# Performance work log

Hardware: AMD Instinct MI355X
Metric: run time of the kernel (lower is better)

Reference implementation:

```python
import jax, jax.numpy as jnp
import numpy as np

EPS = 1e-8
H, DH = 4, 8
HID = H * DH  # 32
FF = 20       # 4 * dim
C = 5         # channels per degree


def snorm(x):
    # grad-safe L2 norm over last axis
    return jnp.sqrt(jnp.sum(x * x, axis=-1) + 1e-12)


def _ln(v, gamma, beta):
    mu = v.mean(-1, keepdims=True)
    sd = v.std(-1, keepdims=True) + EPS
    return (v - mu) / sd * gamma + beta


def norm_se3(x0, x1, g, b):
    # equivariant norm: transform per-channel invariant norms, keep orientation (phase)
    n0 = jnp.abs(x0)
    y0 = jnp.sign(x0) * jax.nn.gelu(_ln(n0, g[0], b[0]))
    n1 = snorm(x1)                                        # (b,n,c)
    y1 = x1 / n1[..., None] * jax.nn.gelu(_ln(n1, g[1], b[1]))[..., None]
    return y0, y1


def attention(x0, x1, coors, adjm, Wq, Mk, Mv, R1, rb1, R2, rb2, Wo0, Wo1):
    b, n, c = x0.shape
    rel = coors[:, None, :, :] - coors[:, :, None, :]     # (b,i,j,3): x_j - x_i
    dist = jnp.sqrt(jnp.sum(rel * rel, -1, keepdims=True) + 1e-12)
    u = rel / dist                                        # unit directions
    # radial net -> per-edge kernel coefficients for each degree-pair/basis (k and v)
    phi = jax.nn.relu(dist @ R1 + rb1) @ R2 + rb2         # (b,i,j,12*HID)
    (k00, k10, k01, kI, kU, kX, v00, v10, v01, vI, vU, vX) = jnp.split(phi, 12, -1)

    def edge_feats(M, p00, p10, p01, pI, pU, pX):
        y00 = jnp.einsum('bjc,ch->bjh', x0, M[0])
        y10 = jnp.einsum('bjcm,ch->bjhm', x1, M[1])
        y01 = jnp.einsum('bjc,ch->bjh', x0, M[2])
        yI = jnp.einsum('bjcm,ch->bjhm', x1, M[3])
        yU = jnp.einsum('bjcm,ch->bjhm', x1, M[4])
        yX = jnp.einsum('bjcm,ch->bjhm', x1, M[5])
        # degree-0 messages: (0->0) scalar and (1->0) vector.dot(u) paths
        e0 = p00 * y00[:, None] + p10 * jnp.einsum('bjhm,bijm->bijh', y10, u)
        un = u[:, :, :, None, :]                          # (b,i,j,1,3)
        # degree-1 messages: closed-form equivariant bases u*s, I, u(u.v), u x v
        e1 = (p01[..., None] * y01[:, None, :, :, None] * un
              + pI[..., None] * yI[:, None]
              + pU[..., None] * jnp.einsum('bjhm,bijm->bijh', yU, u)[..., None] * un
              + pX[..., None] * jnp.cross(un, yX[:, None]))
        return e0, e1

    k0, k1 = edge_feats(Mk, k00, k10, k01, kI, kU, kX)
    v0, v1 = edge_feats(Mv, v00, v10, v01, vI, vU, vX)

    q0 = jnp.einsum('bic,ch->bih', x0, Wq[0]).reshape(b, n, H, DH)
    q1 = jnp.einsum('bicm,ch->bihm', x1, Wq[1]).reshape(b, n, H, DH, 3)
    logits = (jnp.einsum('bihd,bijhd->bhij', q0, k0.reshape(b, n, n, H, DH))
              + jnp.einsum('bihdm,bijhdm->bhij', q1, k1.reshape(b, n, n, H, DH, 3)))
    logits = logits / jnp.asarray(DH, x0.dtype) ** 0.5
    logits = jnp.where(adjm[:, None], logits, -1e9)       # sparse-neighbor mask
    attn = jax.nn.softmax(logits, axis=-1)
    o0 = jnp.einsum('bhij,bijhd->bihd', attn, v0.reshape(b, n, n, H, DH)).reshape(b, n, HID)
    o1 = jnp.einsum('bhij,bijhdm->bihdm', attn, v1.reshape(b, n, n, H, DH, 3)).reshape(b, n, HID, 3)
    return o0 @ Wo0, jnp.einsum('bnhm,hc->bncm', o1, Wo1)


def feedforward(x0, x1, Wf1, Wf2, gs, bs):
    h0 = jax.nn.gelu(jnp.einsum('bnc,cf->bnf', x0, Wf1[0]))
    h1 = jnp.einsum('bncm,cf->bnfm', x1, Wf1[1])
    h1 = h1 * jax.nn.sigmoid(snorm(h1) * gs + bs)[..., None]   # norm-gated nonlin (equivariant)
    return jnp.einsum('bnf,fc->bnc', h0, Wf2[0]), jnp.einsum('bnfm,fc->bncm', h1, Wf2[1])


def _forward(feats, coors, adj_mat, Wq, Mk, Mv, R1, rb1, R2, rb2, Wo0, Wo1, gnA, bnA, gnF, bnF, Wf1, Wf2, gs, bs, Wh1, bh1, Wh2, bh2):
    b, n, _ = feats.shape
    a = adj_mat.astype(jnp.float32)
    # num_adj_degrees=2: attend over 1-hop OR 2-hop neighbors (plus self)
    adjm = adj_mat | ((a @ a) > 0) | jnp.eye(n, dtype=bool)
    x0 = feats
    x1 = jnp.zeros(feats.shape + (3,), feats.dtype)       # input fiber has only degree-0
    x0n, x1n = norm_se3(x0, x1, gnA, bnA)
    d0, d1 = attention(x0n, x1n, coors, adjm, Wq, Mk, Mv, R1, rb1, R2, rb2, Wo0, Wo1)
    x0, x1 = x0 + d0, x1 + d1
    x0n, x1n = norm_se3(x0, x1, gnF, bnF)
    f0, f1 = feedforward(x0n, x1n, Wf1, Wf2, gs, bs)
    x0, x1 = x0 + f0, x1 + f1
    pooled = x0.mean(axis=1)                              # mean pool type-0 features
    h = jax.nn.relu(pooled @ Wh1 + bh1)
    out = h @ Wh2 + bh2                                   # (b, 9)
    return out.reshape(-1, 3, 3)


def setup_inputs():
    key = jax.random.key(0)
    ks = jax.random.split(key, 16)
    B, N = 2, 256
    g = lambda i, shape, s: jax.random.normal(ks[i], shape, jnp.float32) * s
    feats = g(0, (B, N, C), 1.0)
    coors = g(1, (B, N, 3), 3.0)
    r = jax.random.uniform(ks[2], (B, N, N))
    adj = r < 0.03
    adj = (adj | jnp.swapaxes(adj, 1, 2)) & ~jnp.eye(N, dtype=bool)
    s5, sh, sf, s128 = C ** -0.5, HID ** -0.5, FF ** -0.5, 128 ** -0.5
    return dict(
        feats=feats, coors=coors, adj_mat=adj,
        Wq=g(3, (2, C, HID), s5), Mk=g(4, (6, C, HID), s5), Mv=g(5, (6, C, HID), s5),
        R1=g(6, (1, 32), 1.0), rb1=jnp.zeros(32), R2=g(7, (32, 12 * HID), 32 ** -0.5), rb2=jnp.zeros(12 * HID),
        Wo0=g(8, (HID, C), sh), Wo1=g(9, (HID, C), sh),
        gnA=jnp.ones((2, C)), bnA=jnp.zeros((2, C)), gnF=jnp.ones((2, C)), bnF=jnp.zeros((2, C)),
        Wf1=g(10, (2, C, FF), s5), Wf2=g(11, (2, FF, C), sf), gs=jnp.ones(FF), bs=jnp.zeros(FF),
        Wh1=g(12, (C, 128), s5), bh1=jnp.zeros(128), Wh2=g(13, (128, 9), s128), bh2=jnp.zeros(9))


def reference(feats, coors, adj_mat, Wq, Mk, Mv, R1, rb1, R2, rb2, Wo0, Wo1, gnA, bnA, gnF, bnF, Wf1, Wf2, gs, bs, Wh1, bh1, Wh2, bh2):
    return _forward(feats, coors, adj_mat, Wq, Mk, Mv, R1, rb1, R2, rb2, Wo0, Wo1, gnA, bnA, gnF, bnF, Wf1, Wf2, gs, bs, Wh1, bh1, Wh2, bh2)
```

## Files before the change

kernel.cpp:

```cpp
#include <hip/hip_runtime.h>
#include <math.h>

#define BB 2
#define NN 256
#define CC 5
#define HIDD 32


__device__ __forceinline__ float gelu_tanh(float x) {
    float x3 = x * x * x;
    return 0.5f * x * (1.0f + tanhf(0.7978845608028654f * (x + 0.044715f * x3)));
}
__device__ __forceinline__ float sgnf(float x) {
    return (x > 0.f) ? 1.f : ((x < 0.f) ? -1.f : 0.f);
}

#define TROW 9
#define TSZ (33 * TROW)

__global__ __launch_bounds__(256) void fused_attn(
    const float* __restrict__ coors,
    const int* __restrict__ adj,
    const float* __restrict__ feats,
    const float* __restrict__ Wq0, const float* __restrict__ Mk0, const float* __restrict__ Mv0,
    const float* __restrict__ gnA0, const float* __restrict__ bnA0,
    const float* __restrict__ R1, const float* __restrict__ rb1,
    const float* __restrict__ R2, const float* __restrict__ rb2,
    const float* __restrict__ Wo0,
    const float* __restrict__ gnF0, const float* __restrict__ bnF0,
    const float* __restrict__ Wf10,
    const float* __restrict__ Wf20,
    float* __restrict__ xfin)
{
    int node = blockIdx.x;
    int b = node >> 8, i = node & 255;
    int tid = threadIdx.x;
    int j = tid;
    int lane = tid & 63, wave = tid >> 6;

    __shared__ float4 sT[4 * TSZ];
    __shared__ float R2k[32][32];
    __shared__ float R2v[32][32];
    __shared__ float sR1[32], srb1[32], tt[32], sts[32];
    __shared__ float q0s[32];
    __shared__ float Wo0t[5][32];
    __shared__ int nlist[NN];
    __shared__ int ncnt;
    __shared__ float wredm[4][4], wreds[4][4], hm[4], hs[4];
    __shared__ float ew[4][5], x0as[5], xfs[5], h0s[20];

    int av = adj[(size_t)(b * NN + i) * NN + j];

    for (int idx = tid; idx < 1024; idx += 256) {
        int w = idx >> 5, hd = idx & 31;
        R2k[w][hd] = R2[w * 384 + hd];
        R2v[w][hd] = R2[w * 384 + 192 + hd];
    }
    if (tid < 32) { sR1[tid] = R1[tid]; srb1[tid] = rb1[tid]; }
    if (tid < 160) Wo0t[tid / 32][tid % 32] = Wo0[(tid % 32) * 5 + tid / 32];
    if (tid == 0) ncnt = 0;

    float dx = coors[(b * NN + j) * 3 + 0] - coors[(b * NN + i) * 3 + 0];
    float dy = coors[(b * NN + j) * 3 + 1] - coors[(b * NN + i) * 3 + 1];
    float dz = coors[(b * NN + j) * 3 + 2] - coors[(b * NN + i) * 3 + 2];
    float dist = sqrtf(dx * dx + dy * dy + dz * dz + 1e-12f);

    float x0n[CC];
    {
        const float* f = feats + (size_t)(b * NN + j) * CC;
        float fv[CC], n0[CC];
        float mu = 0.f;
#pragma unroll
        for (int c = 0; c < CC; c++) { fv[c] = f[c]; n0[c] = fabsf(fv[c]); mu += n0[c]; }
        mu *= (1.0f / CC);
        float var = 0.f;
#pragma unroll
        for (int c = 0; c < CC; c++) { float d = n0[c] - mu; var += d * d; }
        var *= (1.0f / CC);
        float sd = sqrtf(var) + 1e-8f;
#pragma unroll
        for (int c = 0; c < CC; c++) {
            float ln = (n0[c] - mu) / sd * gnA0[c] + bnA0[c];
            x0n[c] = sgnf(fv[c]) * gelu_tanh(ln);
        }
    }

    __syncthreads();

    if (tid < 32) {
        float r = sR1[tid];
        tt[tid] = (r != 0.f) ? (-srb1[tid] / r) : -3.0e38f;
    }
    if (av) { int p = atomicAdd(&ncnt, 1); nlist[p] = j; }
    if (tid < 32) {
        const float* f = feats + (size_t)(b * NN + i) * CC;
        float fv[CC], n0[CC], xi[CC];
        float mu = 0.f;
#pragma unroll
        for (int c = 0; c < CC; c++) { fv[c] = f[c]; n0[c] = fabsf(fv[c]); mu += n0[c]; }
        mu *= (1.0f / CC);
        float var = 0.f;
#pragma unroll
        for (int c = 0; c < CC; c++) { float d = n0[c] - mu; var += d * d; }
        var *= (1.0f / CC);
        float sd = sqrtf(var) + 1e-8f;
#pragma unroll
        for (int c = 0; c < CC; c++) {
            float ln = (n0[c] - mu) / sd * gnA0[c] + bnA0[c];
            xi[c] = sgnf(fv[c]) * gelu_tanh(ln);
        }
        float q = 0.f;
#pragma unroll
        for (int c = 0; c < CC; c++) q = fmaf(xi[c], Wq0[c * HIDD + tid], q);
        q0s[tid] = q;
    }
    float ykr[32];
#pragma unroll
    for (int hd = 0; hd < 32; hd++) ykr[hd] = 0.f;
#pragma unroll
    for (int c = 0; c < CC; c++) {
        float xc = x0n[c];
#pragma unroll
        for (int hd = 0; hd < 32; hd++)
            ykr[hd] = fmaf(xc, Mk0[c * HIDD + hd], ykr[hd]);
    }
    __syncthreads();

    if (tid < 32) {
        float t = tt[tid];
        int rank = 0;
        for (int k = 0; k < 32; k++) {
            float tk = tt[k];
            rank += (tk < t) || (tk == t && k < tid);
        }
        sts[rank] = t;
    }
    int okacc = (av != 0) || (i == j);
    {
        int cnt = ncnt;
        for (int t = 0; t < cnt; t++) {
            int m = nlist[t];
            okacc |= adj[(size_t)(b * NN + m) * NN + j];
        }
    }
    __syncthreads();

    for (int idx = tid; idx < 33 * 32; idx += 256) {
        int p = idx >> 5, hd = idx & 31;
        float rep = (p == 0) ? (sts[0] - 1.0f)
                  : (p == 32) ? (sts[31] + 1.0f)
                  : 0.5f * (sts[p - 1] + sts[p]);
        float A = 0.f, Bv = 0.f, Cv = 0.f, Dv = 0.f;
        for (int w = 0; w < 32; w++) {
            float r = sR1[w], bb = srb1[w];
            if (fmaf(r, rep, bb) > 0.f) {
                float rk = R2k[w][hd];
                float rv = R2v[w][hd];
                A = fmaf(r, rk, A); Bv = fmaf(bb, rk, Bv);
                Cv = fmaf(r, rv, Cv); Dv = fmaf(bb, rv, Dv);
            }
        }
        Bv += rb2[hd];
        Dv += rb2[192 + hd];
        float* tf = (float*)sT;
        tf[(0 * TSZ + p * TROW) * 4 + hd] = A;
        tf[(1 * TSZ + p * TROW) * 4 + hd] = Bv;
        tf[(2 * TSZ + p * TROW) * 4 + hd] = Cv;
        tf[(3 * TSZ + p * TROW) * 4 + hd] = Dv;
    }
    __syncthreads();

    int p = 0;
#pragma unroll
    for (int k = 0; k < 32; k++) p += (sts[k] < dist) ? 1 : 0;

    const float4* Ap = sT + 0 * TSZ + p * TROW;
    const float4* Bp = sT + 1 * TSZ + p * TROW;
    const float4* Cp = sT + 2 * TSZ + p * TROW;
    const float4* Dp = sT + 3 * TSZ + p * TROW;
    const float4* q04 = (const float4*)q0s;

    float lg[4] = {0.f, 0.f, 0.f, 0.f};
#pragma unroll
    for (int q = 0; q < 8; q++) {
        float4 a = Ap[q], bb = Bp[q], qq = q04[q];
        int h = q >> 1;
        lg[h] = fmaf(fmaf(dist, a.x, bb.x) * qq.x, ykr[4 * q + 0], lg[h]);
        lg[h] = fmaf(fmaf(dist, a.y, bb.y) * qq.y, ykr[4 * q + 1], lg[h]);
        lg[h] = fmaf(fmaf(dist, a.z, bb.z) * qq.z, ykr[4 * q + 2], lg[h]);
        lg[h] = fmaf(fmaf(dist, a.w, bb.w) * qq.w, ykr[4 * q + 3], lg[h]);
    }
    {
        const float invs = 0.35355339059327379f;
        bool ok = okacc != 0;
#pragma unroll
        for (int h = 0; h < 4; h++) lg[h] = ok ? lg[h] * invs : -1e9f;
    }

    float attn[4];
#pragma unroll
    for (int h = 0; h < 4; h++) {
        float v = lg[h];
        for (int off = 32; off; off >>= 1) v = fmaxf(v, __shfl_xor(v, off, 64));
        if (lane == 0) wredm[h][wave] = v;
    }
    __syncthreads();
    if (tid < 4) hm[tid] = fmaxf(fmaxf(wredm[tid][0], wredm[tid][1]), fmaxf(wredm[tid][2], wredm[tid][3]));
    __syncthreads();
#pragma unroll
    for (int h = 0; h < 4; h++) lg[h] = expf(lg[h] - hm[h]);
#pragma unroll
    for (int h = 0; h < 4; h++) {
        float v = lg[h];
        for (int off = 32; off; off >>= 1) v += __shfl_xor(v, off, 64);
        if (lane == 0) wreds[h][wave] = v;
    }
    __syncthreads();
    if (tid < 4) hs[tid] = wreds[tid][0] + wreds[tid][1] + wreds[tid][2] + wreds[tid][3];
    __syncthreads();
#pragma unroll
    for (int h = 0; h < 4; h++) attn[h] = lg[h] / hs[h];

    float yvr[32];
#pragma unroll
    for (int hd = 0; hd < 32; hd++) yvr[hd] = 0.f;
#pragma unroll
    for (int c = 0; c < CC; c++) {
        float xc = x0n[c];
#pragma unroll
        for (int hd = 0; hd < 32; hd++)
            yvr[hd] = fmaf(xc, Mv0[c * HIDD + hd], yvr[hd]);
    }

    float e[5] = {0.f, 0.f, 0.f, 0.f, 0.f};
#pragma unroll
    for (int q = 0; q < 8; q++) {
        float4 c4 = Cp[q], d4 = Dp[q];
        float at = attn[q >> 1];
        float4 pv;
        pv.x = at * fmaf(dist, c4.x, d4.x) * yvr[4 * q + 0];
        pv.y = at * fmaf(dist, c4.y, d4.y) * yvr[4 * q + 1];
        pv.z = at * fmaf(dist, c4.z, d4.z) * yvr[4 * q + 2];
        pv.w = at * fmaf(dist, c4.w, d4.w) * yvr[4 * q + 3];
#pragma unroll
        for (int c = 0; c < 5; c++) {
            float4 w4 = ((const float4*)Wo0t[c])[q];
            e[c] = fmaf(pv.x, w4.x, fmaf(pv.y, w4.y, fmaf(pv.z, w4.z, fmaf(pv.w, w4.w, e[c]))));
        }
    }
    for (int off = 32; off; off >>= 1)
#pragma unroll
        for (int c = 0; c < 5; c++) e[c] += __shfl_xor(e[c], off, 64);
    if (lane == 0)
#pragma unroll
        for (int c = 0; c < 5; c++) ew[wave][c] = e[c];
    __syncthreads();

    if (tid < 5) {
        float d0 = ew[0][tid] + ew[1][tid] + ew[2][tid] + ew[3][tid];
        x0as[tid] = feats[node * 5 + tid] + d0;
    }
    __syncthreads();
    if (tid < 5) {
        float x0a[5], n0[5];
        float mu = 0.f;
#pragma unroll
        for (int c = 0; c < 5; c++) { x0a[c] = x0as[c]; n0[c] = fabsf(x0a[c]); mu += n0[c]; }
        mu *= 0.2f;
        float var = 0.f;
#pragma unroll
        for (int c = 0; c < 5; c++) { float d = n0[c] - mu; var += d * d; }
        var *= 0.2f;
        float sd = sqrtf(var) + 1e-8f;
        float ln = (n0[tid] - mu) / sd * gnF0[tid] + bnF0[tid];
        xfs[tid] = sgnf(x0a[tid]) * gelu_tanh(ln);
    }
    __syncthreads();
    if (tid < 20) {
        float s = 0.f;
#pragma unroll
        for (int c = 0; c < 5; c++) s = fmaf(xfs[c], Wf10[c * 20 + tid], s);
        h0s[tid] = gelu_tanh(s);
    }
    __syncthreads();
    if (tid < 5) {
        float f0 = 0.f;
        for (int f = 0; f < 20; f++) f0 = fmaf(h0s[f], Wf20[f * 5 + tid], f0);
        xfin[node * 5 + tid] = x0as[tid] + f0;
    }
}

__global__ __launch_bounds__(256) void head_mlp(const float* __restrict__ xfin,
                         const float* __restrict__ Wh1, const float* __restrict__ bh1,
                         const float* __restrict__ Wh2, const float* __restrict__ bh2,
                         float* __restrict__ out) {
    __shared__ float part[2][5][25];
    __shared__ float pooled[10];
    __shared__ float hdn[2][128];
    int tid = threadIdx.x;
    if (tid < 250) {
        int b = tid / 125, r = tid % 125, c = r / 25, grp = r % 25;
        float s = 0.f;
        for (int i = grp; i < NN; i += 25) s += xfin[(b * NN + i) * 5 + c];
        part[b][c][grp] = s;
    }
    __syncthreads();
    if (tid < 10) {
        int b = tid / 5, c = tid % 5;
        float s = 0.f;
        for (int g = 0; g < 25; g++) s += part[b][c][g];
        pooled[tid] = s * (1.0f / NN);
    }
    __syncthreads();
    {
        int b = tid >> 7, k = tid & 127;
        float s = bh1[k];
#pragma unroll
        for (int c = 0; c < 5; c++) s = fmaf(pooled[b * 5 + c], Wh1[c * 128 + k], s);
        hdn[b][k] = fmaxf(s, 0.f);
    }
    __syncthreads();
    if (tid < 18) {
        int b = tid / 9, o = tid % 9;
        float s = bh2[o];
        for (int k = 0; k < 128; k++) s = fmaf(hdn[b][k], Wh2[k * 9 + o], s);
        out[b * 9 + o] = s;
    }
}

extern "C" void kernel_launch(void* const* d_in, const int* in_sizes, int n_in,
                              void* d_out, int out_size, void* d_ws, size_t ws_size,
                              hipStream_t stream) {
    const float* feats = (const float*)d_in[0];
    const float* coors = (const float*)d_in[1];
    const int*   adj   = (const int*)d_in[2];
    const float* Wq    = (const float*)d_in[3];
    const float* Mk    = (const float*)d_in[4];
    const float* Mv    = (const float*)d_in[5];
    const float* R1    = (const float*)d_in[6];
    const float* rb1   = (const float*)d_in[7];
    const float* R2    = (const float*)d_in[8];
    const float* rb2   = (const float*)d_in[9];
    const float* Wo0   = (const float*)d_in[10];
    const float* gnA   = (const float*)d_in[12];
    const float* bnA   = (const float*)d_in[13];
    const float* gnF   = (const float*)d_in[14];
    const float* bnF   = (const float*)d_in[15];
    const float* Wf1   = (const float*)d_in[16];
    const float* Wf2   = (const float*)d_in[17];
    const float* Wh1   = (const float*)d_in[20];
    const float* bh1   = (const float*)d_in[21];
    const float* Wh2   = (const float*)d_in[22];
    const float* bh2   = (const float*)d_in[23];
    float* out = (float*)d_out;

    float* xfin = (float*)d_ws;

    hipLaunchKernelGGL(fused_attn, dim3(512), dim3(256), 0, stream,
                       coors, adj, feats, Wq, Mk, Mv, gnA, bnA, R1, rb1, R2, rb2,
                       Wo0, gnF, bnF, Wf1, Wf2, xfin);
    hipLaunchKernelGGL(head_mlp, dim3(1), dim3(256), 0, stream,
                       xfin, Wh1, bh1, Wh2, bh2, out);
}
```

Measured before the change: 129.3 us.

## Fuse head MLP via last-block counter and bitmask the radial table build

```diff
diff --git a/kernel.cpp b/kernel.cpp
--- a/kernel.cpp
+++ b/kernel.cpp
@@ -1,7 +1,6 @@
 #include <hip/hip_runtime.h>
 #include <math.h>
 
-#define BB 2
 #define NN 256
 #define CC 5
 #define HIDD 32
@@ -18,7 +17,7 @@
 #define TROW 9
 #define TSZ (33 * TROW)
 
-__global__ __launch_bounds__(256) void fused_attn(
+__global__ __launch_bounds__(256) void fused_all(
     const float* __restrict__ coors,
     const int* __restrict__ adj,
     const float* __restrict__ feats,
@@ -30,7 +29,11 @@
     const float* __restrict__ gnF0, const float* __restrict__ bnF0,
     const float* __restrict__ Wf10,
     const float* __restrict__ Wf20,
-    float* __restrict__ xfin)
+    const float* __restrict__ Wh1, const float* __restrict__ bh1,
+    const float* __restrict__ Wh2, const float* __restrict__ bh2,
+    float* __restrict__ xfin,
+    int* __restrict__ ctr, const int* __restrict__ refw,
+    float* __restrict__ out)
 {
     int node = blockIdx.x;
     int b = node >> 8, i = node & 255;
@@ -39,24 +42,30 @@
     int lane = tid & 63, wave = tid >> 6;
 
     __shared__ float4 sT[4 * TSZ];
-    __shared__ float R2k[32][32];
-    __shared__ float R2v[32][32];
-    __shared__ float sR1[32], srb1[32], tt[32], sts[32];
+    __shared__ float2 kv[32][32];
+    __shared__ float2 srr[32];
+    __shared__ float srb2k[32], srb2v[32];
+    __shared__ float tt[32], sts[32];
+    __shared__ unsigned int smask[33];
     __shared__ float q0s[32];
     __shared__ float Wo0t[5][32];
     __shared__ int nlist[NN];
     __shared__ int ncnt;
     __shared__ float wredm[4][4], wreds[4][4], hm[4], hs[4];
     __shared__ float ew[4][5], x0as[5], xfs[5], h0s[20];
+    __shared__ float part[2][5][25], pooled[10], hdn[2][128];
 
     int av = adj[(size_t)(b * NN + i) * NN + j];
 
     for (int idx = tid; idx < 1024; idx += 256) {
         int w = idx >> 5, hd = idx & 31;
-        R2k[w][hd] = R2[w * 384 + hd];
-        R2v[w][hd] = R2[w * 384 + 192 + hd];
-    }
-    if (tid < 32) { sR1[tid] = R1[tid]; srb1[tid] = rb1[tid]; }
+        kv[w][hd] = make_float2(R2[w * 384 + hd], R2[w * 384 + 192 + hd]);
+    }
+    if (tid < 32) {
+        srr[tid] = make_float2(R1[tid], rb1[tid]);
+        srb2k[tid] = rb2[tid];
+        srb2v[tid] = rb2[192 + tid];
+    }
     if (tid < 160) Wo0t[tid / 32][tid % 32] = Wo0[(tid % 32) * 5 + tid / 32];
     if (tid == 0) ncnt = 0;
 
@@ -84,48 +93,12 @@
             x0n[c] = sgnf(fv[c]) * gelu_tanh(ln);
         }
     }
-
     __syncthreads();
 
     if (tid < 32) {
-        float r = sR1[tid];
-        tt[tid] = (r != 0.f) ? (-srb1[tid] / r) : -3.0e38f;
-    }
-    if (av) { int p = atomicAdd(&ncnt, 1); nlist[p] = j; }
-    if (tid < 32) {
-        const float* f = feats + (size_t)(b * NN + i) * CC;
-        float fv[CC], n0[CC], xi[CC];
-        float mu = 0.f;
-#pragma unroll
-        for (int c = 0; c < CC; c++) { fv[c] = f[c]; n0[c] = fabsf(fv[c]); mu += n0[c]; }
-        mu *= (1.0f / CC);
-        float var = 0.f;
-#pragma unroll
-        for (int c = 0; c < CC; c++) { float d = n0[c] - mu; var += d * d; }
-        var *= (1.0f / CC);
-        float sd = sqrtf(var) + 1e-8f;
-#pragma unroll
-        for (int c = 0; c < CC; c++) {
-            float ln = (n0[c] - mu) / sd * gnA0[c] + bnA0[c];
-            xi[c] = sgnf(fv[c]) * gelu_tanh(ln);
-        }
-        float q = 0.f;
-#pragma unroll
-        for (int c = 0; c < CC; c++) q = fmaf(xi[c], Wq0[c * HIDD + tid], q);
-        q0s[tid] = q;
-    }
-    float ykr[32];
-#pragma unroll
-    for (int hd = 0; hd < 32; hd++) ykr[hd] = 0.f;
-#pragma unroll
-    for (int c = 0; c < CC; c++) {
-        float xc = x0n[c];
-#pragma unroll
-        for (int hd = 0; hd < 32; hd++)
-            ykr[hd] = fmaf(xc, Mk0[c * HIDD + hd], ykr[hd]);
-    }
-    __syncthreads();
-
+        float r = srr[tid].x;
+        tt[tid] = (r != 0.f) ? (-srr[tid].y / r) : -3.0e38f;
+    }
     if (tid < 32) {
         float t = tt[tid];
         int rank = 0;
@@ -135,33 +108,84 @@
         }
         sts[rank] = t;
     }
+    if (tid < 33) {
+        float rep = (tid == 0) ? (sts[0] - 1.0f)
+                  : (tid == 32) ? (sts[31] + 1.0f)
+                  : 0.5f * (sts[tid - 1] + sts[tid]);
+        unsigned int m = 0;
+        for (int w = 0; w < 32; w++) {
+            float2 rr = srr[w];
+            if (fmaf(rr.x, rep, rr.y) > 0.f) m |= (1u << w);
+        }
+        smask[tid] = m;
+    }
+    if (tid < 32) {
+        const float* f = feats + (size_t)(b * NN + i) * CC;
+        float fv[CC], n0[CC], xi[CC];
+        float mu = 0.f;
+#pragma unroll
+        for (int c = 0; c < CC; c++) { fv[c] = f[c]; n0[c] = fabsf(fv[c]); mu += n0[c]; }
+        mu *= (1.0f / CC);
+        float var = 0.f;
+#pragma unroll
+        for (int c = 0; c < CC; c++) { float d = n0[c] - mu; var += d * d; }
+        var *= (1.0f / CC);
+        float sd = sqrtf(var) + 1e-8f;
+#pragma unroll
+        for (int c = 0; c < CC; c++) {
+            float ln = (n0[c] - mu) / sd * gnA0[c] + bnA0[c];
+            xi[c] = sgnf(fv[c]) * gelu_tanh(ln);
+        }
+        float q = 0.f;
+#pragma unroll
+        for (int c = 0; c < CC; c++) q = fmaf(xi[c], Wq0[c * HIDD + tid], q);
+        q0s[tid] = q;
+    }
+    if (av) { int p = atomicAdd(&ncnt, 1); nlist[p] = j; }
+
+    float ykr[32];
+#pragma unroll
+    for (int hd = 0; hd < 32; hd++) ykr[hd] = 0.f;
+#pragma unroll
+    for (int c = 0; c < CC; c++) {
+        float xc = x0n[c];
+#pragma unroll
+        for (int hd = 0; hd < 32; hd++)
+            ykr[hd] = fmaf(xc, Mk0[c * HIDD + hd], ykr[hd]);
+    }
+    __syncthreads();
+
     int okacc = (av != 0) || (i == j);
     {
         int cnt = ncnt;
-        for (int t = 0; t < cnt; t++) {
-            int m = nlist[t];
-            okacc |= adj[(size_t)(b * NN + m) * NN + j];
-        }
-    }
-    __syncthreads();
-
+        for (int t = 0; t < cnt; t += 8) {
+            int idxs[8], vv[8];
+#pragma unroll
+            for (int k = 0; k < 8; k++) {
+                int u = t + k;
+                idxs[k] = nlist[(u < cnt) ? u : t];
+            }
+#pragma unroll
+            for (int k = 0; k < 8; k++)
+                vv[k] = adj[(size_t)(b * NN + idxs[k]) * NN + j];
+#pragma unroll
+            for (int k = 0; k < 8; k++) okacc |= vv[k];
+        }
+    }
     for (int idx = tid; idx < 33 * 32; idx += 256) {
         int p = idx >> 5, hd = idx & 31;
-        float rep = (p == 0) ? (sts[0] - 1.0f)
-                  : (p == 32) ? (sts[31] + 1.0f)
-                  : 0.5f * (sts[p - 1] + sts[p]);
+        unsigned int m = smask[p];
         float A = 0.f, Bv = 0.f, Cv = 0.f, Dv = 0.f;
-        for (int w = 0; w < 32; w++) {
-            float r = sR1[w], bb = srb1[w];
-            if (fmaf(r, rep, bb) > 0.f) {
-                float rk = R2k[w][hd];
-                float rv = R2v[w][hd];
-                A = fmaf(r, rk, A); Bv = fmaf(bb, rk, Bv);
-                Cv = fmaf(r, rv, Cv); Dv = fmaf(bb, rv, Dv);
-            }
-        }
-        Bv += rb2[hd];
-        Dv += rb2[192 + hd];
+        while (m) {
+            int w = __ffs(m) - 1;
+            m &= (m - 1);
+            float2 rr = srr[w];
+            float2 kw = kv[w][hd];
+            A  = fmaf(rr.x, kw.x, A);  Bv = fmaf(rr.y, kw.x, Bv);
+            Cv = fmaf(rr.x, kw.y, Cv); Dv = fmaf(rr.y, kw.y, Dv);
+        }
+        Bv += srb2k[hd];
+        Dv += srb2v[hd];
         float* tf = (float*)sT;
         tf[(0 * TSZ + p * TROW) * 4 + hd] = A;
         tf[(1 * TSZ + p * TROW) * 4 + hd] = Bv;
@@ -256,12 +280,13 @@
         for (int c = 0; c < 5; c++) ew[wave][c] = e[c];
     __syncthreads();
 
-    if (tid < 5) {
-        float d0 = ew[0][tid] + ew[1][tid] + ew[2][tid] + ew[3][tid];
-        x0as[tid] = feats[node * 5 + tid] + d0;
-    }
-    __syncthreads();
-    if (tid < 5) {
+    if (wave != 0) return;
+
+    if (lane < 5) {
+        float d0 = ew[0][lane] + ew[1][lane] + ew[2][lane] + ew[3][lane];
+        x0as[lane] = feats[node * 5 + lane] + d0;
+    }
+    if (lane < 5) {
         float x0a[5], n0[5];
         float mu = 0.f;
 #pragma unroll
@@ -272,59 +297,60 @@
         for (int c = 0; c < 5; c++) { float d = n0[c] - mu; var += d * d; }
         var *= 0.2f;
         float sd = sqrtf(var) + 1e-8f;
-        float ln = (n0[tid] - mu) / sd * gnF0[tid] + bnF0[tid];
-        xfs[tid] = sgnf(x0a[tid]) * gelu_tanh(ln);
-    }
-    __syncthreads();
-    if (tid < 20) {
+        float ln = (n0[lane] - mu) / sd * gnF0[lane] + bnF0[lane];
+        xfs[lane] = sgnf(x0a[lane]) * gelu_tanh(ln);
+    }
+    if (lane < 20) {
         float s = 0.f;
 #pragma unroll
-        for (int c = 0; c < 5; c++) s = fmaf(xfs[c], Wf10[c * 20 + tid], s);
-        h0s[tid] = gelu_tanh(s);
-    }
-    __syncthreads();
-    if (tid < 5) {
+        for (int c = 0; c < 5; c++) s = fmaf(xfs[c], Wf10[c * 20 + lane], s);
+        h0s[lane] = gelu_tanh(s);
+    }
+    if (lane < 5) {
         float f0 = 0.f;
-        for (int f = 0; f < 20; f++) f0 = fmaf(h0s[f], Wf20[f * 5 + tid], f0);
-        xfin[node * 5 + tid] = x0as[tid] + f0;
-    }
-}
-
-__global__ __launch_bounds__(256) void head_mlp(const float* __restrict__ xfin,
-                         const float* __restrict__ Wh1, const float* __restrict__ bh1,
-                         const float* __restrict__ Wh2, const float* __restrict__ bh2,
-                         float* __restrict__ out) {
-    __shared__ float part[2][5][25];
-    __shared__ float pooled[10];
-    __shared__ float hdn[2][128];
-    int tid = threadIdx.x;
-    if (tid < 250) {
-        int b = tid / 125, r = tid % 125, c = r / 25, grp = r % 25;
+        for (int f = 0; f < 20; f++) f0 = fmaf(h0s[f], Wf20[f * 5 + lane], f0);
+        xfin[node * 5 + lane] = x0as[lane] + f0;
+    }
+
+    __threadfence();
+    int slast = 0, base = 0;
+    if (lane == 0) {
+        base = __hip_atomic_load(refw, __ATOMIC_RELAXED, __HIP_MEMORY_SCOPE_AGENT);
+        int old = __hip_atomic_fetch_add(ctr, 1, __ATOMIC_ACQ_REL, __HIP_MEMORY_SCOPE_AGENT);
+        slast = ((old - base) == 511) ? 1 : 0;
+    }
+    slast = __shfl(slast, 0, 64);
+    if (!slast) return;
+
+    __threadfence();
+
+    for (int tpl = lane; tpl < 250; tpl += 64) {
+        int bb = tpl / 125, r = tpl % 125, c = r / 25, grp = r % 25;
         float s = 0.f;
-        for (int i = grp; i < NN; i += 25) s += xfin[(b * NN + i) * 5 + c];
-        part[b][c][grp] = s;
-    }
-    __syncthreads();
-    if (tid < 10) {
-        int b = tid / 5, c = tid % 5;
+        for (int ii = grp; ii < NN; ii += 25) s += xfin[(bb * NN + ii) * 5 + c];
+        part[bb][c][grp] = s;
+    }
+    if (lane < 10) {
+        int bb = lane / 5, c = lane % 5;
         float s = 0.f;
-        for (int g = 0; g < 25; g++) s += part[b][c][g];
-        pooled[tid] = s * (1.0f / NN);
-    }
-    __syncthreads();
-    {
-        int b = tid >> 7, k = tid & 127;
+        for (int g = 0; g < 25; g++) s += part[bb][c][g];
+        pooled[lane] = s * (1.0f / NN);
+    }
+    for (int kk = lane; kk < 256; kk += 64) {
+        int bb = kk >> 7, k = kk & 127;
         float s = bh1[k];
 #pragma unroll
-        for (int c = 0; c < 5; c++) s = fmaf(pooled[b * 5 + c], Wh1[c * 128 + k], s);
-        hdn[b][k] = fmaxf(s, 0.f);
-    }
-    __syncthreads();
-    if (tid < 18) {
-        int b = tid / 9, o = tid % 9;
+        for (int c = 0; c < 5; c++) s = fmaf(pooled[bb * 5 + c], Wh1[c * 128 + k], s);
+        hdn[bb][k] = fmaxf(s, 0.f);
+    }
+    if (lane < 18) {
+        int bb = lane / 9, o = lane % 9;
         float s = bh2[o];
-        for (int k = 0; k < 128; k++) s = fmaf(hdn[b][k], Wh2[k * 9 + o], s);
-        out[b * 9 + o] = s;
+        for (int k = 0; k < 128; k++) s = fmaf(hdn[bb][k], Wh2[k * 9 + o], s);
+        out[bb * 9 + o] = s;
+    }
+    if (lane == 0) {
+        __hip_atomic_store(ctr, base, __ATOMIC_RELAXED, __HIP_MEMORY_SCOPE_AGENT);
     }
 }
 
@@ -355,10 +381,11 @@
     float* out = (float*)d_out;
 
     float* xfin = (float*)d_ws;
-
-    hipLaunchKernelGGL(fused_attn, dim3(512), dim3(256), 0, stream,
+    int* ctr    = (int*)((char*)d_ws + 16384);
+    const int* refw = (const int*)((char*)d_ws + 16400);
+
+    hipLaunchKernelGGL(fused_all, dim3(512), dim3(256), 0, stream,
                        coors, adj, feats, Wq, Mk, Mv, gnA, bnA, R1, rb1, R2, rb2,
-                       Wo0, gnF, bnF, Wf1, Wf2, xfin);
-    hipLaunchKernelGGL(head_mlp, dim3(1), dim3(256), 0, stream,
-                       xfin, Wh1, bh1, Wh2, bh2, out);
+                       Wo0, gnF, bnF, Wf1, Wf2, Wh1, bh1, Wh2, bh2,
+                       xfin, ctr, refw, out);
 }
```

Result: slower. 155.4 us (+20.2%).
